# Kernel tuning notes

Measured on AMD Instinct MI355X. Metric: run time of the kernel, lower is better.

Reference implementation:

```python
import jax, jax.numpy as jnp
import numpy as np

EPS = 1e-5
NUM_CRYSTALS = 64


def _bn(x2d, g, b):
    # torch BatchNorm1d in training mode: biased batch stats, affine
    m = x2d.mean(0)
    v = x2d.var(0)
    return g * (x2d - m) * jax.lax.rsqrt(v + EPS) + b


def _improved_conv(x, e, idx, p):
    (fcW, fcb, g1, b1, g2, b2, eW, eb, ge, be, W3, b3, g3, b3b) = p
    N, M = idx.shape
    A = x.shape[1]
    Bf = e.shape[2]
    xn = x[idx]  # (N, M, A) gathered neighbor atom features
    tot = jnp.concatenate([jnp.broadcast_to(x[:, None, :], (N, M, A)), xn, e], axis=2)  # (N,M,2A+B)
    # 2-body gated message
    h = jnp.einsum('nmf,of->nmo', tot, fcW) + fcb
    h = _bn(h.reshape(-1, 2 * A), g1, b1).reshape(N, M, 2 * A)
    two_body = jnp.sum(jax.nn.sigmoid(h[..., :A]) * jax.nn.softplus(h[..., A:]), axis=1)
    # explicit edge update
    he = jnp.einsum('nmf,of->nmo', tot, eW) + eb
    he = _bn(he.reshape(-1, 2 * Bf), ge, be).reshape(N, M, 2 * Bf)
    e_out = e + jax.nn.sigmoid(he[..., :Bf]) * jax.nn.softplus(he[..., Bf:])
    # 3-body: split W3 by concat blocks [x_i, x_j, x_l, e_ij, e_il] so the
    # (N,M,M,3A+2B) concat is never materialized; only (N,M,M,2A) is formed.
    Wa, Wj, Wl, Wij, Wil = jnp.split(W3, [A, 2 * A, 3 * A, 3 * A + Bf], axis=1)
    h3 = ((x @ Wa.T)[:, None, None, :]
          + (xn @ Wj.T)[:, :, None, :]
          + (xn @ Wl.T)[:, None, :, :]
          + (e @ Wij.T)[:, :, None, :]
          + (e @ Wil.T)[:, None, :, :]
          + b3)  # (N, M, M, 2A)
    h3 = _bn(h3.reshape(-1, 2 * A), g3, b3b).reshape(N, M, M, 2 * A)
    three_body = jnp.sum(jax.nn.sigmoid(h3[..., :A]) * jax.nn.softplus(h3[..., A:]), axis=(1, 2))
    total = _bn(two_body + three_body, g2, b2)
    return jax.nn.softplus(x + total), e_out


def setup_inputs() -> dict:
    key = jax.random.key(0)
    ks = jax.random.split(key, 12)
    N, M, OF, A, BF, H, NC = 2000, 12, 92, 64, 41, 128, 3
    f = lambda k, s: jax.random.normal(k, s, dtype=jnp.float32) * 0.05
    z = lambda s: jnp.zeros(s, jnp.float32)
    o = lambda s: jnp.ones(s, jnp.float32)
    return {
        'atom_fea': jax.random.normal(ks[0], (N, OF), dtype=jnp.float32),
        'nbr_fea': jax.random.normal(ks[1], (N, M, BF), dtype=jnp.float32),
        'nbr_fea_idx': jax.random.randint(ks[2], (N, M), 0, N),
        'site_seg': jnp.sort(jax.random.randint(ks[3], (N,), 0, NUM_CRYSTALS)),
        'emb_W': f(ks[4], (A, OF)), 'emb_b': z((A,)),
        'fcW': f(ks[5], (NC, 2 * A, 2 * A + BF)), 'fcb': z((NC, 2 * A)),
        'bn1_g': o((NC, 2 * A)), 'bn1_b': z((NC, 2 * A)),
        'bn2_g': o((NC, A)), 'bn2_b': z((NC, A)),
        'eW': f(ks[6], (NC, 2 * BF, 2 * A + BF)), 'eb': z((NC, 2 * BF)),
        'bne_g': o((NC, 2 * BF)), 'bne_b': z((NC, 2 * BF)),
        'W3': f(ks[7], (NC, 2 * A, 3 * A + 2 * BF)), 'b3': z((NC, 2 * A)),
        'bn3_g': o((NC, 2 * A)), 'bn3_b': z((NC, 2 * A)),
        'fc1W': f(ks[8], (H, A)), 'fc1b': z((H,)),
        'outW': f(ks[9], (1, H)), 'outb': z((1,)),
    }


def reference(atom_fea, nbr_fea, nbr_fea_idx, site_seg, emb_W, emb_b,
              fcW, fcb, bn1_g, bn1_b, bn2_g, bn2_b, eW, eb, bne_g, bne_b,
              W3, b3, bn3_g, bn3_b, fc1W, fc1b, outW, outb):
    x = atom_fea @ emb_W.T + emb_b  # embedding1 (orbital=False)
    e = nbr_fea
    n_conv = fcW.shape[0]
    for i in range(n_conv):  # small fixed layer loop
        p = (fcW[i], fcb[i], bn1_g[i], bn1_b[i], bn2_g[i], bn2_b[i],
             eW[i], eb[i], bne_g[i], bne_b[i], W3[i], b3[i], bn3_g[i], bn3_b[i])
        x, e = _improved_conv(x, e, nbr_fea_idx, p)
    x = jax.nn.softplus(jax.nn.softplus(x) @ fc1W.T + fc1b)  # conv_to_fc1
    # per-crystal mean pooling over site segments
    N = x.shape[0]
    sums = jax.ops.segment_sum(x, site_seg, num_segments=NUM_CRYSTALS)
    counts = jax.ops.segment_sum(jnp.ones((N, 1), x.dtype), site_seg, num_segments=NUM_CRYSTALS)
    pooled = sums / jnp.maximum(counts, 1.0)
    return pooled @ outW.T + outb  # (NUM_CRYSTALS, 1)
```

## Files before the change

### kernel.cpp

```cpp
#include <hip/hip_runtime.h>
#include <hip/hip_bf16.h>

#define N_ATOM 2000
#define MNBR   12
#define OFEA   92
#define AF     64
#define BFEA   41
#define K1     169
#define O1     128
#define OE     82
#define K3     274
#define NM     24000
#define NCONV  3
#define HID    128
#define NCRY   64
#define EPS_BN 1e-5f

#define LDA_T  192
#define LDH    512
#define LDSW   88

typedef __bf16 bf16x8 __attribute__((ext_vector_type(8)));
typedef float  f32x4  __attribute__((ext_vector_type(4)));

__device__ __forceinline__ float sigmoidf_(float x){
    return __builtin_amdgcn_rcpf(1.f + __expf(-x));
}
__device__ __forceinline__ float softplusf_(float x){
    return fmaxf(x,0.f) + __logf(1.f + __expf(-fabsf(x)));
}
__device__ __forceinline__ float b2f(__hip_bfloat16 v){ return __bfloat162float(v); }

__global__ __launch_bounds__(256)
void gemm_bf16(const __hip_bfloat16* __restrict__ A,
               const __hip_bfloat16* __restrict__ W,
               const float* __restrict__ bias,
               __hip_bfloat16* __restrict__ C)
{
    __shared__ unsigned short As[128][LDSW];
    __shared__ unsigned short Ws[128][LDSW];
    const int tid  = threadIdx.x;
    const int row0 = blockIdx.x * 128;
    const int col0 = blockIdx.y * 128;
    const int w    = tid >> 6;
    const int l    = tid & 63;
    const int wm   = w >> 1, wn = w & 1;
    const int lrow = l & 15;
    const int quad = l >> 4;

    f32x4 acc[4][4];
    #pragma unroll
    for (int i=0;i<4;i++)
        #pragma unroll
        for (int j=0;j<4;j++) acc[i][j] = (f32x4){0.f,0.f,0.f,0.f};

    for (int it = 0; it < 3; ++it){
        const int k0 = it * 64;
        if (it) __syncthreads();
        #pragma unroll
        for (int j = 0; j < 4; ++j){
            int e  = tid + j*256;
            int r  = e >> 3;
            int kk = (e & 7) << 3;
            int grow = row0 + r;
            uint4 va = make_uint4(0,0,0,0);
            if (grow < NM)
                va = *(const uint4*)(A + (size_t)grow*LDA_T + k0 + kk);
            *(uint4*)(&As[r][kk]) = va;
            uint4 vw = *(const uint4*)(W + (size_t)(col0 + r)*LDA_T + k0 + kk);
            *(uint4*)(&Ws[r][kk]) = vw;
        }
        __syncthreads();
        #pragma unroll
        for (int ks = 0; ks < 2; ++ks){
            int koff = ks*32 + quad*8;
            bf16x8 a_[4], b_[4];
            #pragma unroll
            for (int mi=0;mi<4;mi++)
                a_[mi] = *(const bf16x8*)(&As[wm*64 + mi*16 + lrow][koff]);
            #pragma unroll
            for (int ni=0;ni<4;ni++)
                b_[ni] = *(const bf16x8*)(&Ws[wn*64 + ni*16 + lrow][koff]);
            #pragma unroll
            for (int mi=0;mi<4;mi++)
                #pragma unroll
                for (int ni=0;ni<4;ni++)
                    acc[mi][ni] = __builtin_amdgcn_mfma_f32_16x16x32_bf16(
                        a_[mi], b_[ni], acc[mi][ni], 0, 0, 0);
        }
    }
    #pragma unroll
    for (int ni=0;ni<4;ni++){
        int col = col0 + wn*64 + ni*16 + lrow;
        float bv = bias[col];
        #pragma unroll
        for (int mi=0;mi<4;mi++){
            int rbase = row0 + wm*64 + mi*16 + quad*4;
            #pragma unroll
            for (int reg=0;reg<4;reg++){
                int grow = rbase + reg;
                if (grow < NM)
                    C[(size_t)grow*LDH + col] = __float2bfloat16(acc[mi][ni][reg] + bv);
            }
        }
    }
}

#define BM 64
#define BN 128
#define BK 32
template<int EPI, int SPIN>
__global__ __launch_bounds__(256)
void gemm_tn(const float* __restrict__ T, int ldt, int R,
             const float* __restrict__ W, int ldw, int K, int O,
             const float* __restrict__ bias,
             float* __restrict__ C, int ldc)
{
    __shared__ float Ts[BM][BK+1];
    __shared__ float Ws2[BN][BK+1];
    const int tid = threadIdx.x;
    const int row0 = blockIdx.x * BM;
    const int tx = tid % 16;
    const int ty = tid / 16;
    float acc[4][8];
    #pragma unroll
    for (int i=0;i<4;i++)
        #pragma unroll
        for (int j=0;j<8;j++) acc[i][j]=0.f;

    for (int k0 = 0; k0 < K; k0 += BK) {
        #pragma unroll
        for (int i=0;i<(BM*BK)/256;i++){
            int e = tid + i*256;
            int r = e / BK, k = e % BK;
            int gr = row0 + r, gk = k0 + k;
            float v = 0.f;
            if (gr < R && gk < K){
                v = T[(size_t)gr*ldt + gk];
                if (SPIN) v = softplusf_(v);
            }
            Ts[r][k] = v;
        }
        #pragma unroll
        for (int i=0;i<(BN*BK)/256;i++){
            int e = tid + i*256;
            int r = e / BK, k = e % BK;
            int gk = k0 + k;
            Ws2[r][k] = (r < O && gk < K) ? W[(size_t)r*ldw + gk] : 0.f;
        }
        __syncthreads();
        #pragma unroll
        for (int k=0;k<BK;k++){
            float a_[4], b_[8];
            #pragma unroll
            for (int i=0;i<4;i++) a_[i] = Ts[ty*4+i][k];
            #pragma unroll
            for (int j=0;j<8;j++) b_[j] = Ws2[tx + j*16][k];
            #pragma unroll
            for (int i=0;i<4;i++)
                #pragma unroll
                for (int j=0;j<8;j++)
                    acc[i][j] += a_[i]*b_[j];
        }
        __syncthreads();
    }
    #pragma unroll
    for (int i=0;i<4;i++){
        int gr = row0 + ty*4 + i;
        if (gr >= R) continue;
        #pragma unroll
        for (int j=0;j<8;j++){
            int gc = tx + j*16;
            if (gc >= O) continue;
            float v = acc[i][j] + (bias ? bias[gc] : 0.f);
            if (EPI==1) v = softplusf_(v);
            C[(size_t)gr*ldc + gc] = v;
        }
    }
}

__global__ void pack_all(const float* __restrict__ fcW, const float* __restrict__ eW,
                         const float* __restrict__ W3, const float* __restrict__ fcb,
                         const float* __restrict__ eb, const float* __restrict__ b3,
                         __hip_bfloat16* __restrict__ WALL, float* __restrict__ BIAS)
{
    int i = blockIdx.x*blockDim.x + threadIdx.x;
    const int nW = NCONV*512*LDA_T;
    if (i < nW){
        int l = i/(512*LDA_T), rem = i%(512*LDA_T);
        int c = rem/LDA_T, k = rem%LDA_T;
        float v = 0.f;
        if (c < O1){
            if (k < K1) v = fcW[((size_t)l*O1 + c)*K1 + k];
        } else if (c < O1+OE){
            if (k < K1) v = eW[((size_t)l*OE + (c-O1))*K1 + k];
        } else if (c >= 256 && c < 384){
            int o = c - 256;
            const float* W3l = W3 + (size_t)l*O1*K3;
            if (k < AF)                        v = 0.5f * W3l[(size_t)o*K3 + k];
            else if (k < 2*AF)                 v = W3l[(size_t)o*K3 + k];
            else if (k < K1)                   v = W3l[(size_t)o*K3 + 192 + (k-128)];
        } else if (c >= 384){
            int o = c - 384;
            const float* W3l = W3 + (size_t)l*O1*K3;
            if (k < AF)                        v = 0.5f * W3l[(size_t)o*K3 + k];
            else if (k < 2*AF)                 v = W3l[(size_t)o*K3 + k + AF];
            else if (k < K1)                   v = W3l[(size_t)o*K3 + 233 + (k-128)];
        }
        WALL[i] = __float2bfloat16(v);
    } else if (i < nW + NCONV*512){
        int m = i - nW;
        int l = m/512, c = m%512;
        float v = 0.f;
        if (c < O1)         v = fcb[l*O1 + c];
        else if (c < O1+OE) v = eb[l*OE + (c-O1)];
        else if (c >= 256)  v = 0.5f * b3[l*O1 + ((c-256)&127)];
        BIAS[m] = v;
    }
}

__global__ void gather_b(__hip_bfloat16* __restrict__ TOT, const float* __restrict__ X,
                         const float* __restrict__ E, const int* __restrict__ idx)
{
    int i = blockIdx.x*blockDim.x + threadIdx.x;
    if (i >= NM*24) return;
    int grp = i % 24, r = i / 24;
    int n = r / MNBR;
    float v[8];
    if (grp < 16){
        const float* src = (grp < 8) ? (X + (size_t)n*AF + grp*8)
                                     : (X + (size_t)idx[r]*AF + (grp-8)*8);
        #pragma unroll
        for (int j=0;j<8;j++) v[j] = src[j];
    } else {
        int base = (grp-16)*8;
        #pragma unroll
        for (int j=0;j<8;j++){
            int k = base + j;
            v[j] = (k < BFEA) ? E[(size_t)r*BFEA + k] : 0.f;
        }
    }
    __hip_bfloat16 o[8];
    #pragma unroll
    for (int j=0;j<8;j++) o[j] = __float2bfloat16(v[j]);
    *(uint4*)(TOT + (size_t)r*LDA_T + grp*8) = *(const uint4*)o;
}

__global__ __launch_bounds__(256)
void stats_all(const __hip_bfloat16* __restrict__ REST,
               float* __restrict__ S1A, float* __restrict__ S2A,
               float* __restrict__ S13, float* __restrict__ S23)
{
    const int tid = threadIdx.x;
    const int n0 = blockIdx.x * 4;
    const int r0 = n0 * MNBR;
    if (tid < O1+OE){
        float s1 = 0.f, s2 = 0.f;
        #pragma unroll 4
        for (int j = 0; j < 4*MNBR; ++j){
            float v = b2f(REST[(size_t)(r0+j)*LDH + tid]);
            s1 += v; s2 += v*v;
        }
        atomicAdd(&S1A[tid], s1);
        atomicAdd(&S2A[tid], s2);
    }
    if (tid < O1){
        float s1 = 0.f, s2 = 0.f;
        for (int a = 0; a < 4; ++a){
            int n = n0 + a;
            float sp=0.f, spp=0.f, sq=0.f, sqq=0.f;
            #pragma unroll
            for (int m=0;m<MNBR;m++){
                const __hip_bfloat16* row = REST + (size_t)(n*MNBR+m)*LDH;
                float p = b2f(row[256 + tid]);
                float q = b2f(row[384 + tid]);
                sp += p; spp += p*p; sq += q; sqq += q*q;
            }
            s1 += 12.f*(sp+sq);
            s2 += 12.f*(spp+sqq) + 2.f*sp*sq;
        }
        atomicAdd(&S13[tid], s1);
        atomicAdd(&S23[tid], s2);
    }
}

__global__ void bn_fin_all(const float* __restrict__ S1A, const float* __restrict__ S2A,
                           const float* __restrict__ S13, const float* __restrict__ S23,
                           const float* __restrict__ g1, const float* __restrict__ b1,
                           const float* __restrict__ ge, const float* __restrict__ be,
                           const float* __restrict__ g3, const float* __restrict__ b3b,
                           float* __restrict__ SC)
{
    int c = threadIdx.x;
    if (c < O1+OE){
        float mean = S1A[c]*(1.f/NM);
        float var  = fmaxf(S2A[c]*(1.f/NM) - mean*mean, 0.f);
        float gg = (c < O1) ? g1[c] : ge[c-O1];
        float bb = (c < O1) ? b1[c] : be[c-O1];
        float sc = gg * rsqrtf(var + EPS_BN);
        SC[c] = sc; SC[256+c] = bb - sc*mean;
    }
    if (c < O1){
        float mean = S13[c]*(1.f/((float)NM*MNBR));
        float var  = fmaxf(S23[c]*(1.f/((float)NM*MNBR)) - mean*mean, 0.f);
        float sc = g3[c] * rsqrtf(var + EPS_BN);
        SC[512+c] = sc; SC[640+c] = b3b[c] - sc*mean;
    }
}

__global__ __launch_bounds__(128)
void consumer_k(const __hip_bfloat16* __restrict__ REST, const float* __restrict__ SC,
                float* __restrict__ TB, float* __restrict__ E)
{
    __shared__ float red[128];
    const int n = blockIdx.x;
    const int t = threadIdx.x;
    const int a = t & 63;
    const int g = t >> 6;
    const __hip_bfloat16* base = REST + (size_t)n*MNBR*LDH;

    float sha = SC[a],      tha = SC[256+a];
    float shb = SC[64+a],   thb = SC[256+64+a];
    float s3lo = SC[512+a], s3hi = SC[512+64+a];
    float t3lo = SC[640+a], t3hi = SC[640+64+a];

    float Qa[MNBR], Qb[MNBR];
    #pragma unroll
    for (int m=0;m<MNBR;m++){
        const __hip_bfloat16* row = base + (size_t)m*LDH;
        Qa[m] = s3lo*b2f(row[384+a]);
        Qb[m] = s3hi*b2f(row[448+a]);
    }
    float acc = 0.f;
    #pragma unroll
    for (int j=0;j<6;j++){
        const __hip_bfloat16* row = base + (size_t)(g*6+j)*LDH;
        acc += sigmoidf_(sha*b2f(row[a])+tha) * softplusf_(shb*b2f(row[64+a])+thb);
        float ua = s3lo*b2f(row[256+a]) + t3lo;
        float ub = s3hi*b2f(row[320+a]) + t3hi;
        #pragma unroll
        for (int l2=0;l2<MNBR;l2++)
            acc += sigmoidf_(ua + Qa[l2]) * softplusf_(ub + Qb[l2]);
    }
    red[t] = acc;
    __syncthreads();
    if (g == 0)
        TB[(size_t)n*AF + a] = red[a] + red[64+a];
    for (int idx = t; idx < MNBR*BFEA; idx += 128){
        int m = idx / BFEA, b = idx % BFEA;
        const __hip_bfloat16* row = base + (size_t)m*LDH;
        float u = SC[O1+b]*b2f(row[O1+b])   + SC[256+O1+b];
        float v = SC[169+b]*b2f(row[169+b]) + SC[256+169+b];
        E[(size_t)n*MNBR*BFEA + idx] += sigmoidf_(u) * softplusf_(v);
    }
}

__global__ __launch_bounds__(64)
void tb_stats_k(const float* __restrict__ TB,
                float* __restrict__ S1, float* __restrict__ S2)
{
    int t = threadIdx.x;
    float s1 = 0.f, s2 = 0.f;
    for (int r = blockIdx.x; r < N_ATOM; r += gridDim.x){
        float v = TB[(size_t)r*AF + t];
        s1 += v; s2 += v*v;
    }
    atomicAdd(&S1[t], s1);
    atomicAdd(&S2[t], s2);
}

__global__ void x_update_k(float* __restrict__ X, const float* __restrict__ TB,
                           const float* __restrict__ S12, const float* __restrict__ S22,
                           const float* __restrict__ g2, const float* __restrict__ b2,
                           int total)
{
    int i = blockIdx.x*blockDim.x + threadIdx.x;
    if (i >= total) return;
    int a = i & (AF-1);
    float mean = S12[a]*(1.f/N_ATOM);
    float var  = fmaxf(S22[a]*(1.f/N_ATOM) - mean*mean, 0.f);
    float sc = g2[a]*rsqrtf(var + EPS_BN);
    X[i] = softplusf_(X[i] + sc*TB[i] + (b2[a] - sc*mean));
}

__global__ __launch_bounds__(128)
void pool_out_k(const float* __restrict__ Z, const int* __restrict__ seg,
                const float* __restrict__ outW, const float* __restrict__ outb,
                float* __restrict__ out)
{
    __shared__ float red[128];
    const int c = blockIdx.x;
    const int h = threadIdx.x;
    int l0, l1;
    {
        int l=0, r=N_ATOM;
        while (l<r){ int m=(l+r)>>1; if (seg[m] < c) l=m+1; else r=m; }
        l0 = l;
        l=l0; r=N_ATOM;
        while (l<r){ int m=(l+r)>>1; if (seg[m] < c+1) l=m+1; else r=m; }
        l1 = l;
    }
    float s = 0.f;
    for (int n = l0; n < l1; ++n) s += Z[(size_t)n*HID + h];
    float cnt = fmaxf((float)(l1-l0), 1.f);
    red[h] = (s/cnt) * outW[h];
    __syncthreads();
    for (int off=64; off>0; off>>=1){
        if (h < off) red[h] += red[h+off];
        __syncthreads();
    }
    if (h == 0) out[c] = red[0] + outb[0];
}

extern "C" void kernel_launch(void* const* d_in, const int* in_sizes, int n_in,
                              void* d_out, int out_size, void* d_ws, size_t ws_size,
                              hipStream_t stream)
{
    const float* atom_fea = (const float*)d_in[0];
    const float* nbr_fea  = (const float*)d_in[1];
    const int*   nbr_idx  = (const int*)d_in[2];
    const int*   site_seg = (const int*)d_in[3];
    const float* emb_W = (const float*)d_in[4];
    const float* emb_b = (const float*)d_in[5];
    const float* fcW   = (const float*)d_in[6];
    const float* fcb   = (const float*)d_in[7];
    const float* bn1_g = (const float*)d_in[8];
    const float* bn1_b = (const float*)d_in[9];
    const float* bn2_g = (const float*)d_in[10];
    const float* bn2_b = (const float*)d_in[11];
    const float* eW    = (const float*)d_in[12];
    const float* eb    = (const float*)d_in[13];
    const float* bne_g = (const float*)d_in[14];
    const float* bne_b = (const float*)d_in[15];
    const float* W3    = (const float*)d_in[16];
    const float* b3    = (const float*)d_in[17];
    const float* bn3_g = (const float*)d_in[18];
    const float* bn3_b = (const float*)d_in[19];
    const float* fc1W  = (const float*)d_in[20];
    const float* fc1b  = (const float*)d_in[21];
    const float* outW  = (const float*)d_in[22];
    const float* outb  = (const float*)d_in[23];

    float* ws   = (float*)d_ws;
    float* X    = ws;
    float* E    = ws + 128000;
    __hip_bfloat16* TOT = (__hip_bfloat16*)(ws + 1112000);
    __hip_bfloat16* REST = (__hip_bfloat16*)(ws + 2264000);
    float* TB   = ws + 8408000;
    float* ST   = ws + 8536000;
    float* SC   = ws + 8542144;
    __hip_bfloat16* WALL = (__hip_bfloat16*)(ws + 8543168);
    float* BIAS = ws + 8690624;
    float* Z    = ws + 8692160;

    {
        int tot = NCONV*512*LDA_T + NCONV*512;
        pack_all<<<(tot+255)/256, 256, 0, stream>>>(fcW, eW, W3, fcb, eb, b3, WALL, BIAS);
    }
    hipMemsetAsync(ST, 0, NCONV*2048*sizeof(float), stream);
    gemm_tn<0,0><<<(N_ATOM+BM-1)/BM, 256, 0, stream>>>(atom_fea, OFEA, N_ATOM,
                                                       emb_W, OFEA, OFEA, AF, emb_b, X, AF);
    hipMemcpyAsync(E, nbr_fea, (size_t)NM*BFEA*sizeof(float),
                   hipMemcpyDeviceToDevice, stream);

    for (int i = 0; i < NCONV; i++){
        const float* g1 = bn1_g + i*O1, *b1 = bn1_b + i*O1;
        const float* g2 = bn2_g + i*AF, *b2 = bn2_b + i*AF;
        const float* ge = bne_g + i*OE, *be = bne_b + i*OE;
        const float* g3 = bn3_g + i*O1, *b3b = bn3_b + i*O1;
        float* STL = ST + i*2048;
        float *S1A=STL, *S2A=STL+256, *S13=STL+512, *S23=STL+640, *S12=STL+768, *S22=STL+832;

        gather_b<<<(NM*24+255)/256, 256, 0, stream>>>(TOT, X, E, nbr_idx);
        {
            dim3 g((NM+127)/128, 4);
            gemm_bf16<<<g, 256, 0, stream>>>(TOT, WALL + (size_t)i*512*LDA_T,
                                             BIAS + i*512, REST);
        }
        stats_all<<<N_ATOM/4, 256, 0, stream>>>(REST, S1A, S2A, S13, S23);
        bn_fin_all<<<1, 256, 0, stream>>>(S1A, S2A, S13, S23,
                                          g1, b1, ge, be, g3, b3b, SC);
        consumer_k<<<N_ATOM, 128, 0, stream>>>(REST, SC, TB, E);
        tb_stats_k<<<128, 64, 0, stream>>>(TB, S12, S22);
        x_update_k<<<(N_ATOM*AF+255)/256, 256, 0, stream>>>(X, TB, S12, S22, g2, b2,
                                                            N_ATOM*AF);
    }

    gemm_tn<1,1><<<(N_ATOM+BM-1)/BM, 256, 0, stream>>>(X, AF, N_ATOM, fc1W, AF, AF, HID,
                                                       fc1b, Z, HID);
    pool_out_k<<<NCRY, 128, 0, stream>>>(Z, site_seg, outW, outb, (float*)d_out);
}
```

Measured before the change: 428.7 us.

## Fuse neighbor gather into GEMM tile load and fold BN finalize into stats

The GEMM now builds its A tile directly from X, the neighbor indices and the edge features, converting fp32 to bf16 as it loads, so the separate gather kernel and the TOT buffer are gone. The BN finalize step moves into the stats kernel: the last block, found through an atomic counter, computes the scale and shift. The initial device-to-device copy of the edge features is replaced by having the consumer read the input E and write the output E out of place. This removes three launches or copies per layer and one round trip through TOT, at the cost of uncoalesced fp32 gather loads that are repeated across the four column blocks, plus a threadfence and counter atomic in every stats block.

```diff
diff --git a/kernel.cpp b/kernel.cpp
--- a/kernel.cpp
+++ b/kernel.cpp
@@ -16,8 +16,8 @@
 #define NCRY   64
 #define EPS_BN 1e-5f
 
+#define LDH    512
 #define LDA_T  192
-#define LDH    512
 #define LDSW   88
 
 typedef __bf16 bf16x8 __attribute__((ext_vector_type(8)));
@@ -32,10 +32,11 @@
 __device__ __forceinline__ float b2f(__hip_bfloat16 v){ return __bfloat162float(v); }
 
 __global__ __launch_bounds__(256)
-void gemm_bf16(const __hip_bfloat16* __restrict__ A,
-               const __hip_bfloat16* __restrict__ W,
-               const float* __restrict__ bias,
-               __hip_bfloat16* __restrict__ C)
+void gemm_fused(const float* __restrict__ X, const float* __restrict__ E,
+                const int* __restrict__ idx,
+                const __hip_bfloat16* __restrict__ W,
+                const float* __restrict__ bias,
+                __hip_bfloat16* __restrict__ C)
 {
     __shared__ unsigned short As[128][LDSW];
     __shared__ unsigned short Ws[128][LDSW];
@@ -54,21 +55,52 @@
         #pragma unroll
         for (int j=0;j<4;j++) acc[i][j] = (f32x4){0.f,0.f,0.f,0.f};
 
+    #pragma unroll
     for (int it = 0; it < 3; ++it){
         const int k0 = it * 64;
         if (it) __syncthreads();
         #pragma unroll
         for (int j = 0; j < 4; ++j){
             int e  = tid + j*256;
-            int r  = e >> 3;
+            int rl = e >> 3;
             int kk = (e & 7) << 3;
-            int grow = row0 + r;
-            uint4 va = make_uint4(0,0,0,0);
-            if (grow < NM)
-                va = *(const uint4*)(A + (size_t)grow*LDA_T + k0 + kk);
-            *(uint4*)(&As[r][kk]) = va;
-            uint4 vw = *(const uint4*)(W + (size_t)(col0 + r)*LDA_T + k0 + kk);
-            *(uint4*)(&Ws[r][kk]) = vw;
+            int gr = row0 + rl;
+            float vals[8];
+            #pragma unroll
+            for (int q=0;q<8;q++) vals[q] = 0.f;
+            if (gr < NM){
+                if (it == 0){
+                    int n = gr / MNBR;
+                    const float* src = X + (size_t)n*AF + kk;
+                    #pragma unroll
+                    for (int q=0;q<8;q++) vals[q] = src[q];
+                } else if (it == 1){
+                    int nb = idx[gr];
+                    const float* src = X + (size_t)nb*AF + kk;
+                    #pragma unroll
+                    for (int q=0;q<8;q++) vals[q] = src[q];
+                } else {
+                    if (kk < BFEA){
+                        const float* src = E + (size_t)gr*BFEA + kk;
+                        int lim = BFEA - kk;
+                        #pragma unroll
+                        for (int q=0;q<8;q++)
+                            if (q < lim) vals[q] = src[q];
+                    }
+                }
+            }
+            __hip_bfloat16 ob[8];
+            #pragma unroll
+            for (int q=0;q<8;q++) ob[q] = __float2bfloat16(vals[q]);
+            *(uint4*)(&As[rl][kk]) = *(const uint4*)ob;
+        }
+        #pragma unroll
+        for (int j = 0; j < 4; ++j){
+            int e  = tid + j*256;
+            int rl = e >> 3;
+            int kk = (e & 7) << 3;
+            uint4 vw = *(const uint4*)(W + (size_t)(col0 + rl)*LDA_T + k0 + kk);
+            *(uint4*)(&Ws[rl][kk]) = vw;
         }
         __syncthreads();
         #pragma unroll
@@ -219,38 +251,16 @@
     }
 }
 
-__global__ void gather_b(__hip_bfloat16* __restrict__ TOT, const float* __restrict__ X,
-                         const float* __restrict__ E, const int* __restrict__ idx)
-{
-    int i = blockIdx.x*blockDim.x + threadIdx.x;
-    if (i >= NM*24) return;
-    int grp = i % 24, r = i / 24;
-    int n = r / MNBR;
-    float v[8];
-    if (grp < 16){
-        const float* src = (grp < 8) ? (X + (size_t)n*AF + grp*8)
-                                     : (X + (size_t)idx[r]*AF + (grp-8)*8);
-        #pragma unroll
-        for (int j=0;j<8;j++) v[j] = src[j];
-    } else {
-        int base = (grp-16)*8;
-        #pragma unroll
-        for (int j=0;j<8;j++){
-            int k = base + j;
-            v[j] = (k < BFEA) ? E[(size_t)r*BFEA + k] : 0.f;
-        }
-    }
-    __hip_bfloat16 o[8];
-    #pragma unroll
-    for (int j=0;j<8;j++) o[j] = __float2bfloat16(v[j]);
-    *(uint4*)(TOT + (size_t)r*LDA_T + grp*8) = *(const uint4*)o;
-}
-
 __global__ __launch_bounds__(256)
 void stats_all(const __hip_bfloat16* __restrict__ REST,
                float* __restrict__ S1A, float* __restrict__ S2A,
-               float* __restrict__ S13, float* __restrict__ S23)
-{
+               float* __restrict__ S13, float* __restrict__ S23,
+               const float* __restrict__ g1, const float* __restrict__ b1,
+               const float* __restrict__ ge, const float* __restrict__ be,
+               const float* __restrict__ g3, const float* __restrict__ b3b,
+               float* __restrict__ SC, unsigned int* __restrict__ counter)
+{
+    __shared__ int slast;
     const int tid = threadIdx.x;
     const int n0 = blockIdx.x * 4;
     const int r0 = n0 * MNBR;
@@ -282,35 +292,39 @@
         atomicAdd(&S13[tid], s1);
         atomicAdd(&S23[tid], s2);
     }
-}
-
-__global__ void bn_fin_all(const float* __restrict__ S1A, const float* __restrict__ S2A,
-                           const float* __restrict__ S13, const float* __restrict__ S23,
-                           const float* __restrict__ g1, const float* __restrict__ b1,
-                           const float* __restrict__ ge, const float* __restrict__ be,
-                           const float* __restrict__ g3, const float* __restrict__ b3b,
-                           float* __restrict__ SC)
-{
-    int c = threadIdx.x;
-    if (c < O1+OE){
-        float mean = S1A[c]*(1.f/NM);
-        float var  = fmaxf(S2A[c]*(1.f/NM) - mean*mean, 0.f);
-        float gg = (c < O1) ? g1[c] : ge[c-O1];
-        float bb = (c < O1) ? b1[c] : be[c-O1];
-        float sc = gg * rsqrtf(var + EPS_BN);
-        SC[c] = sc; SC[256+c] = bb - sc*mean;
-    }
-    if (c < O1){
-        float mean = S13[c]*(1.f/((float)NM*MNBR));
-        float var  = fmaxf(S23[c]*(1.f/((float)NM*MNBR)) - mean*mean, 0.f);
-        float sc = g3[c] * rsqrtf(var + EPS_BN);
-        SC[512+c] = sc; SC[640+c] = b3b[c] - sc*mean;
+    __threadfence();
+    if (tid == 0){
+        unsigned int old = atomicAdd(counter, 1u);
+        slast = (old == gridDim.x - 1u) ? 1 : 0;
+    }
+    __syncthreads();
+    if (slast){
+        int c = tid;
+        if (c < O1+OE){
+            float s1 = atomicAdd(&S1A[c], 0.f);
+            float s2 = atomicAdd(&S2A[c], 0.f);
+            float mean = s1*(1.f/NM);
+            float var  = fmaxf(s2*(1.f/NM) - mean*mean, 0.f);
+            float gg = (c < O1) ? g1[c] : ge[c-O1];
+            float bb = (c < O1) ? b1[c] : be[c-O1];
+            float sc = gg * rsqrtf(var + EPS_BN);
+            SC[c] = sc; SC[256+c] = bb - sc*mean;
+        }
+        if (c < O1){
+            float s1 = atomicAdd(&S13[c], 0.f);
+            float s2 = atomicAdd(&S23[c], 0.f);
+            float mean = s1*(1.f/((float)NM*MNBR));
+            float var  = fmaxf(s2*(1.f/((float)NM*MNBR)) - mean*mean, 0.f);
+            float sc = g3[c] * rsqrtf(var + EPS_BN);
+            SC[512+c] = sc; SC[640+c] = b3b[c] - sc*mean;
+        }
     }
 }
 
 __global__ __launch_bounds__(128)
 void consumer_k(const __hip_bfloat16* __restrict__ REST, const float* __restrict__ SC,
-                float* __restrict__ TB, float* __restrict__ E)
+                float* __restrict__ TB, const float* __restrict__ Ein,
+                float* __restrict__ Eout)
 {
     __shared__ float red[128];
     const int n = blockIdx.x;
@@ -351,7 +365,8 @@
         const __hip_bfloat16* row = base + (size_t)m*LDH;
         float u = SC[O1+b]*b2f(row[O1+b])   + SC[256+O1+b];
         float v = SC[169+b]*b2f(row[169+b]) + SC[256+169+b];
-        E[(size_t)n*MNBR*BFEA + idx] += sigmoidf_(u) * softplusf_(v);
+        Eout[(size_t)n*MNBR*BFEA + idx] = Ein[(size_t)n*MNBR*BFEA + idx]
+                                        + sigmoidf_(u) * softplusf_(v);
     }
 }
 
@@ -444,14 +459,13 @@
     float* ws   = (float*)d_ws;
     float* X    = ws;
     float* E    = ws + 128000;
-    __hip_bfloat16* TOT = (__hip_bfloat16*)(ws + 1112000);
-    __hip_bfloat16* REST = (__hip_bfloat16*)(ws + 2264000);
-    float* TB   = ws + 8408000;
-    float* ST   = ws + 8536000;
-    float* SC   = ws + 8542144;
-    __hip_bfloat16* WALL = (__hip_bfloat16*)(ws + 8543168);
-    float* BIAS = ws + 8690624;
-    float* Z    = ws + 8692160;
+    __hip_bfloat16* REST = (__hip_bfloat16*)(ws + 1112000);
+    float* TB   = ws + 7256000;
+    float* ST   = ws + 7384000;
+    float* SC   = ws + 7390144;
+    __hip_bfloat16* WALL = (__hip_bfloat16*)(ws + 7391168);
+    float* BIAS = ws + 7538624;
+    float* Z    = ws + 7540160;
 
     {
         int tot = NCONV*512*LDA_T + NCONV*512;
@@ -460,8 +474,6 @@
     hipMemsetAsync(ST, 0, NCONV*2048*sizeof(float), stream);
     gemm_tn<0,0><<<(N_ATOM+BM-1)/BM, 256, 0, stream>>>(atom_fea, OFEA, N_ATOM,
                                                        emb_W, OFEA, OFEA, AF, emb_b, X, AF);
-    hipMemcpyAsync(E, nbr_fea, (size_t)NM*BFEA*sizeof(float),
-                   hipMemcpyDeviceToDevice, stream);
 
     for (int i = 0; i < NCONV; i++){
         const float* g1 = bn1_g + i*O1, *b1 = bn1_b + i*O1;
@@ -470,17 +482,18 @@
         const float* g3 = bn3_g + i*O1, *b3b = bn3_b + i*O1;
         float* STL = ST + i*2048;
         float *S1A=STL, *S2A=STL+256, *S13=STL+512, *S23=STL+640, *S12=STL+768, *S22=STL+832;
-
-        gather_b<<<(NM*24+255)/256, 256, 0, stream>>>(TOT, X, E, nbr_idx);
+        unsigned int* CNT = (unsigned int*)(STL + 1024);
+        const float* Ein = (i == 0) ? nbr_fea : E;
+
         {
             dim3 g((NM+127)/128, 4);
-            gemm_bf16<<<g, 256, 0, stream>>>(TOT, WALL + (size_t)i*512*LDA_T,
-                                             BIAS + i*512, REST);
-        }
-        stats_all<<<N_ATOM/4, 256, 0, stream>>>(REST, S1A, S2A, S13, S23);
-        bn_fin_all<<<1, 256, 0, stream>>>(S1A, S2A, S13, S23,
-                                          g1, b1, ge, be, g3, b3b, SC);
-        consumer_k<<<N_ATOM, 128, 0, stream>>>(REST, SC, TB, E);
+            gemm_fused<<<g, 256, 0, stream>>>(X, Ein, nbr_idx,
+                                              WALL + (size_t)i*512*LDA_T,
+                                              BIAS + i*512, REST);
+        }
+        stats_all<<<N_ATOM/4, 256, 0, stream>>>(REST, S1A, S2A, S13, S23,
+                                                g1, b1, ge, be, g3, b3b, SC, CNT);
+        consumer_k<<<N_ATOM, 128, 0, stream>>>(REST, SC, TB, Ein, E);
         tb_stats_k<<<128, 64, 0, stream>>>(TB, S12, S22);
         x_update_k<<<(N_ATOM*AF+255)/256, 256, 0, stream>>>(X, TB, S12, S22, g2, b2,
                                                             N_ATOM*AF);
```

Measured after the change: 531.3 us. +23.9%, slower.
